# Kernel tuning notes

Measured on AMD Instinct MI355X. Metric: run time of the kernel, lower is better.

The kernel has to match this reference:

```python
import jax, jax.numpy as jnp
import numpy as np

B, S = 1, 8192
QC = 4096          # query_channels
H = 64             # num_heads (== key_channels == output_channels, forced by forward body)
KC = 64            # key_channels
OC = 64            # output_channels
P = 0.25           # dropout prob


def setup_inputs() -> dict:
    key = jax.random.key(0)
    ks = jax.random.split(key, 8)
    w = lambda k, shape: jax.random.normal(k, shape, dtype=jnp.float32) * 0.02
    return {
        "query": jax.random.normal(ks[0], (B, S, QC), dtype=jnp.float32),
        "key_in": jax.random.normal(ks[1], (B, S, KC), dtype=jnp.float32),
        "value": jax.random.normal(ks[2], (B, S, KC), dtype=jnp.float32),
        "mask_u": jax.random.uniform(ks[3], (B, S, H, H), dtype=jnp.float32),
        # Linear weights stored (in, out); torch stores (out, in) but math is identical.
        "Wq": w(ks[4], (QC, H * KC)), "bq": jnp.zeros((H * KC,), jnp.float32),
        "Wk": w(ks[5], (KC, H * KC)), "bk": jnp.zeros((H * KC,), jnp.float32),
        "Wv": w(ks[6], (KC, H * OC)), "bv": jnp.zeros((H * OC,), jnp.float32),
        "Wo": w(ks[7], (H * OC, OC)), "bo": jnp.zeros((OC,), jnp.float32),
    }


def reference(query, key_in, value, mask_u, Wq, bq, Wk, bk, Wv, bv, Wo, bo):
    # Projections
    q = (query @ Wq + bq).reshape(B, S, H, KC)
    k = (key_in @ Wk + bk).reshape(B, S, H, KC)
    v = (value @ Wv + bv).reshape(B, S, H, KC)   # source views v with key_channels (Oc==Kc)
    # transpose(-2, -1): (B, S, KC, H)
    qT = jnp.swapaxes(q, -2, -1)
    kT = jnp.swapaxes(k, -2, -1)
    vT = jnp.swapaxes(v, -2, -1)
    # Per-token 'attention': contracts H of qT against KC of kT (H == KC). No sqrt(d) scale.
    attn_logits = jnp.matmul(qT, kT)             # (B, S, H, H)
    # safe_logsoftmax: numerically stable log-softmax (NOT softmax) over last dim
    attn = jax.nn.log_softmax(attn_logits, axis=-1)
    # dropout p=0.25, deterministic via precomputed uniforms
    keep = (mask_u > P).astype(attn.dtype) / (1.0 - P)
    attn = attn * keep
    out = jnp.matmul(attn, vT)                   # (B, S, H, H)
    # transpose(0,1) -> (S, B, H, H), then view(S, -1) -> (S, B*H*H) with B==1
    out = jnp.swapaxes(out, 0, 1).reshape(S, -1)
    return out @ Wo + bo                          # (S, OC)
```

## Files before the change

### kernel.cpp

```cpp
#include <hip/hip_runtime.h>
#include <stdint.h>
#include <stddef.h>

typedef unsigned short u16;
typedef __bf16 bf16x8 __attribute__((ext_vector_type(8)));
typedef float f32x4 __attribute__((ext_vector_type(4)));

#define DEVINL __device__ __forceinline__

DEVINL u16 f2bf(float f) {
  uint32_t u = __builtin_bit_cast(uint32_t, f);
  u += 0x7FFFu + ((u >> 16) & 1u);
  return (u16)(u >> 16);
}
DEVINL float bf2f(u16 h) {
  uint32_t u = ((uint32_t)h) << 16;
  return __builtin_bit_cast(float, u);
}
DEVINL uint32_t pack2(float a, float b) {
  return (uint32_t)f2bf(a) | ((uint32_t)f2bf(b) << 16);
}

DEVINL void gload_lds16(const u16* g, u16* lds) {
  __builtin_amdgcn_global_load_lds(
      (const __attribute__((address_space(1))) uint32_t*)g,
      (__attribute__((address_space(3))) uint32_t*)lds, 16, 0, 0);
}

__global__ __launch_bounds__(256) void cast_kernel(const float* __restrict__ x,
                                                   u16* __restrict__ y, int n8) {
  int i = blockIdx.x * 256 + threadIdx.x;
  if (i >= n8) return;
  const float4* xp = (const float4*)x + (size_t)i * 2;
  float4 a = xp[0], b = xp[1];
  uint4 o;
  o.x = pack2(a.x, a.y);
  o.y = pack2(a.z, a.w);
  o.z = pack2(b.x, b.y);
  o.w = pack2(b.z, b.w);
  ((uint4*)y)[i] = o;
}

__global__ __launch_bounds__(256) void transpose_cast(const float* __restrict__ W,
                                                      u16* __restrict__ Bt,
                                                      int K, int N) {
  __shared__ float tile[64][65];
  const int nb = blockIdx.x << 6, kb = blockIdx.y << 6;
  const int t = threadIdx.x;
  {
    const int kr = t >> 2, n0 = (t & 3) << 4;
    const float* src = W + (size_t)(kb + kr) * N + nb + n0;
#pragma unroll
    for (int i = 0; i < 16; i += 4) {
      float4 v = *(const float4*)(src + i);
      tile[n0 + i + 0][kr] = v.x;
      tile[n0 + i + 1][kr] = v.y;
      tile[n0 + i + 2][kr] = v.z;
      tile[n0 + i + 3][kr] = v.w;
    }
  }
  __syncthreads();
  {
    const int nr = t >> 2, k0 = (t & 3) << 4;
    u16* dst = Bt + (size_t)(nb + nr) * K + kb + k0;
#pragma unroll
    for (int i = 0; i < 16; i += 8) {
      uint4 o;
      o.x = pack2(tile[nr][k0 + i + 0], tile[nr][k0 + i + 1]);
      o.y = pack2(tile[nr][k0 + i + 2], tile[nr][k0 + i + 3]);
      o.z = pack2(tile[nr][k0 + i + 4], tile[nr][k0 + i + 5]);
      o.w = pack2(tile[nr][k0 + i + 6], tile[nr][k0 + i + 7]);
      *(uint4*)(dst + i) = o;
    }
  }
}

template <int BM, int BN, int WM, int WN, bool OUTF32, bool SPLITK>
__global__ __launch_bounds__(256) void gemm_bf16t(const u16* __restrict__ A,
                                                  const u16* __restrict__ Bt,
                                                  const float* __restrict__ bias,
                                                  void* __restrict__ Cv,
                                                  int M, int N, int K,
                                                  int lda, int ldb) {
  static_assert(WM * WN == 4, "4 waves");
  constexpr int BK = 32;
  constexpr int FM = BM / (WM * 16);
  constexpr int FN = BN / (WN * 16);
  __shared__ __align__(16) u16 Al[BM * BK];
  __shared__ __align__(16) u16 Bl[BN * BK];
  const int t = threadIdx.x;
  const int lane = t & 63, w = t >> 6;
  const int wm = w / WN, wn = w % WN;

  int bn;
  float* Cpart = nullptr;
  if (SPLITK) {
    const int chunk = blockIdx.x;
    A  += (size_t)chunk * K;
    Bt += (size_t)chunk * K;
    Cpart = (float*)Cv + (size_t)chunk * M * N;
    bn = 0;
  } else {
    bn = blockIdx.x * BN;
  }
  const int bm = blockIdx.y * BM;
  const int r16 = lane & 15, khi = lane >> 4;

  f32x4 acc[FM][FN] = {};

  const int srow = t >> 2;
  const int skel = (t & 3) << 3;

  for (int k0 = 0; k0 < K; k0 += BK) {
#pragma unroll
    for (int r = 0; r < BM / 64; ++r) {
      const u16* g = A + (size_t)(bm + r * 64 + srow) * lda + k0 + skel;
      gload_lds16(g, Al + r * 2048 + (w << 9));
    }
#pragma unroll
    for (int r = 0; r < BN / 64; ++r) {
      const u16* g = Bt + (size_t)(bn + r * 64 + srow) * ldb + k0 + skel;
      gload_lds16(g, Bl + r * 2048 + (w << 9));
    }
    __syncthreads();

    bf16x8 af[FM], bfr[FN];
#pragma unroll
    for (int mi = 0; mi < FM; ++mi)
      af[mi] = *(const bf16x8*)(Al + (wm * FM * 16 + mi * 16 + r16) * BK + khi * 8);
#pragma unroll
    for (int ni = 0; ni < FN; ++ni)
      bfr[ni] = *(const bf16x8*)(Bl + (wn * FN * 16 + ni * 16 + r16) * BK + khi * 8);
#pragma unroll
    for (int mi = 0; mi < FM; ++mi)
#pragma unroll
      for (int ni = 0; ni < FN; ++ni)
        acc[mi][ni] = __builtin_amdgcn_mfma_f32_16x16x32_bf16(af[mi], bfr[ni],
                                                              acc[mi][ni], 0, 0, 0);
    __syncthreads();
  }

  const int crow0 = bm + wm * FM * 16 + (khi << 2);
  const int ccol0 = bn + wn * FN * 16 + r16;
#pragma unroll
  for (int mi = 0; mi < FM; ++mi) {
#pragma unroll
    for (int ni = 0; ni < FN; ++ni) {
      const int col = ccol0 + ni * 16;
      const float bv = (!SPLITK && bias) ? bias[col] : 0.0f;
#pragma unroll
      for (int e = 0; e < 4; ++e) {
        const int row = crow0 + mi * 16 + e;
        const float v = acc[mi][ni][e] + bv;
        if (SPLITK)
          Cpart[(size_t)row * N + col] = v;
        else if (OUTF32)
          ((float*)Cv)[(size_t)row * N + col] = v;
        else
          ((u16*)Cv)[(size_t)row * N + col] = f2bf(v);
      }
    }
  }
}

__global__ __launch_bounds__(512, 2) void gemm256(const u16* __restrict__ A,
                                                  const u16* __restrict__ Bt,
                                                  const float* __restrict__ bias,
                                                  u16* __restrict__ C,
                                                  int M, int N, int K) {
  __shared__ __align__(16) u16 LDSu[65536];
  const int t = threadIdx.x;
  const int lane = t & 63, w = t >> 6;
  const int wm = w >> 2, wn = w & 3;
  const int r16 = lane & 15, khi = lane >> 4;
  const int bm = blockIdx.y << 8, bn = blockIdx.x << 8;
  const int nt = K >> 6;

  const int srow = t >> 3;
  const int scb = ((((t & 7) << 4) ^ (((t >> 3) & 7) << 4)) >> 1);

  auto ISSUE_HALF = [&](int tile_, int h_) {
    if (tile_ >= nt) return;
    const int k0_ = tile_ << 6;
    u16* lb_ = LDSu + ((tile_ & 1) << 15) + ((h_ & 2) << 13) + ((h_ & 1) << 13)
               + t * 8;
    const int row0_ = ((h_ & 1) << 7) + srow;
    if (h_ < 2) {
      gload_lds16(A + (size_t)(bm + row0_) * K + k0_ + scb, lb_);
      gload_lds16(A + (size_t)(bm + row0_ + 64) * K + k0_ + scb, lb_ + 4096);
    } else {
      gload_lds16(Bt + (size_t)(bn + row0_) * K + k0_ + scb, lb_);
      gload_lds16(Bt + (size_t)(bn + row0_ + 64) * K + k0_ + scb, lb_ + 4096);
    }
  };

  f32x4 acc[8][4] = {};
  bf16x8 bf[4][2];

  ISSUE_HALF(0, 0);
  ISSUE_HALF(0, 2);
  ISSUE_HALF(0, 3);
  ISSUE_HALF(0, 1);
  ISSUE_HALF(1, 0);
  asm volatile("s_waitcnt vmcnt(4)" ::: "memory");
  __builtin_amdgcn_s_barrier();

  for (int n = 0; n < nt; ++n) {
    const u16* bufb = LDSu + ((n & 1) << 15);
#pragma unroll
    for (int q = 0; q < 4; ++q) {
      bf16x8 af[2][2];
      if (q == 0) {
#pragma unroll
        for (int ni = 0; ni < 4; ++ni)
#pragma unroll
          for (int ks = 0; ks < 2; ++ks)
            bf[ni][ks] = *(const bf16x8*)(bufb + 16384 +
                (64 * wn + 16 * ni + r16) * 64 +
                ((((ks << 6) + (khi << 4)) ^ ((r16 & 7) << 4)) >> 1));
      }
#pragma unroll
      for (int mi2 = 0; mi2 < 2; ++mi2)
#pragma unroll
        for (int ks = 0; ks < 2; ++ks)
          af[mi2][ks] = *(const bf16x8*)(bufb +
              (32 * (2 * q + mi2) + 16 * wm + r16) * 64 +
              ((((ks << 6) + (khi << 4)) ^ ((r16 & 7) << 4)) >> 1));
      __builtin_amdgcn_sched_barrier(0);
      if (q == 0)      ISSUE_HALF(n + 1, 2);
      else if (q == 1) ISSUE_HALF(n + 1, 3);
      else if (q == 2) ISSUE_HALF(n + 1, 1);
      else             ISSUE_HALF(n + 2, 0);
      __builtin_amdgcn_sched_barrier(0);
      __builtin_amdgcn_s_barrier();
      asm volatile("s_waitcnt lgkmcnt(0)" ::: "memory");
      __builtin_amdgcn_sched_barrier(0);
      __builtin_amdgcn_s_setprio(1);
#pragma unroll
      for (int mi2 = 0; mi2 < 2; ++mi2)
#pragma unroll
        for (int ni = 0; ni < 4; ++ni)
#pragma unroll
          for (int ks = 0; ks < 2; ++ks)
            acc[2 * q + mi2][ni] = __builtin_amdgcn_mfma_f32_16x16x32_bf16(
                af[mi2][ks], bf[ni][ks], acc[2 * q + mi2][ni], 0, 0, 0);
      __builtin_amdgcn_s_setprio(0);
      __builtin_amdgcn_sched_barrier(0);
      if (q == 1) {
        if (n < nt - 1)
          asm volatile("s_waitcnt vmcnt(6)" ::: "memory");
        else
          asm volatile("s_waitcnt vmcnt(0)" ::: "memory");
      }
      if (q == 3 && n < nt - 1) {
        if (n < nt - 2)
          asm volatile("s_waitcnt vmcnt(4)" ::: "memory");
        else
          asm volatile("s_waitcnt vmcnt(2)" ::: "memory");
      }
      __builtin_amdgcn_s_barrier();
    }
  }

#pragma unroll
  for (int mi = 0; mi < 8; ++mi) {
    const int row = bm + 32 * mi + 16 * wm + (khi << 2);
#pragma unroll
    for (int ni = 0; ni < 4; ++ni) {
      const int col = bn + 64 * wn + 16 * ni + r16;
      const float bv = bias[col];
#pragma unroll
      for (int e = 0; e < 4; ++e)
        C[(size_t)(row + e) * N + col] = f2bf(acc[mi][ni][e] + bv);
    }
  }
}

__global__ __launch_bounds__(256) void reduce_splitk(const float* __restrict__ part,
                                                     const float* __restrict__ bo,
                                                     float* __restrict__ out, int n) {
  int i = blockIdx.x * 256 + threadIdx.x;
  if (i >= n) return;
  float s = 0.0f;
#pragma unroll
  for (int c = 0; c < 8; ++c) s += part[(size_t)c * 524288 + i];
  out[i] = s + bo[i & 63];
}

__global__ __launch_bounds__(256) void attn_mfma(const u16* __restrict__ Q,
                                                 const u16* __restrict__ Kp,
                                                 const u16* __restrict__ Vp,
                                                 const float* __restrict__ mask,
                                                 u16* __restrict__ OUT) {
  constexpr int LDP = 72;
  __shared__ __align__(16) u16 Pbuf[4][64 * LDP];
  const int t = threadIdx.x;
  const int w = t >> 6, lane = t & 63;
  const int r16 = lane & 15, khi = lane >> 4;
  const int s = blockIdx.x * 4 + w;
  const size_t base = (size_t)s << 12;
  u16* pb = Pbuf[w];

  {
    uint4 rowv[8];
    const uint4* qp = (const uint4*)(Q + base + (size_t)lane * 64);
#pragma unroll
    for (int i = 0; i < 8; ++i) rowv[i] = qp[i];
#pragma unroll
    for (int i = 0; i < 8; ++i) {
      const uint32_t* wp = (const uint32_t*)&rowv[i];
#pragma unroll
      for (int h = 0; h < 4; ++h) {
        uint32_t v = wp[h];
        pb[(8 * i + 2 * h) * LDP + lane] = (u16)(v & 0xffffu);
        pb[(8 * i + 2 * h + 1) * LDP + lane] = (u16)(v >> 16);
      }
    }
  }
  asm volatile("s_waitcnt lgkmcnt(0)" ::: "memory");

  f32x4 acc[4][4] = {};
#pragma unroll
  for (int ks = 0; ks < 2; ++ks) {
    bf16x8 af[4], bfr[4];
#pragma unroll
    for (int mi = 0; mi < 4; ++mi)
      af[mi] = *(const bf16x8*)(pb + (16 * mi + r16) * LDP + ks * 32 + khi * 8);
#pragma unroll
    for (int ni = 0; ni < 4; ++ni)
      bfr[ni] = *(const bf16x8*)(Kp + base + (size_t)(16 * ni + r16) * 64 +
                                 ks * 32 + khi * 8);
#pragma unroll
    for (int mi = 0; mi < 4; ++mi)
#pragma unroll
      for (int ni = 0; ni < 4; ++ni)
        acc[mi][ni] = __builtin_amdgcn_mfma_f32_16x16x32_bf16(af[mi], bfr[ni],
                                                              acc[mi][ni], 0, 0, 0);
  }

  float L[4][4];
#pragma unroll
  for (int mi = 0; mi < 4; ++mi) {
#pragma unroll
    for (int e = 0; e < 4; ++e) {
      float mx = fmaxf(fmaxf(acc[mi][0][e], acc[mi][1][e]),
                       fmaxf(acc[mi][2][e], acc[mi][3][e]));
      mx = fmaxf(mx, __shfl_xor(mx, 1));
      mx = fmaxf(mx, __shfl_xor(mx, 2));
      mx = fmaxf(mx, __shfl_xor(mx, 4));
      mx = fmaxf(mx, __shfl_xor(mx, 8));
      float sm = __expf(acc[mi][0][e] - mx) + __expf(acc[mi][1][e] - mx) +
                 __expf(acc[mi][2][e] - mx) + __expf(acc[mi][3][e] - mx);
      sm += __shfl_xor(sm, 1);
      sm += __shfl_xor(sm, 2);
      sm += __shfl_xor(sm, 4);
      sm += __shfl_xor(sm, 8);
      L[mi][e] = mx + __logf(sm);
    }
  }

  const float* mrow = mask + base;
#pragma unroll
  for (int mi = 0; mi < 4; ++mi) {
#pragma unroll
    for (int ni = 0; ni < 4; ++ni) {
#pragma unroll
      for (int e = 0; e < 4; ++e) {
        const int c = 16 * mi + 4 * khi + e;
        const int j = 16 * ni + r16;
        const float keep = mrow[(size_t)c * 64 + j] > 0.25f ? (1.0f / 0.75f) : 0.0f;
        pb[c * LDP + j] = f2bf((acc[mi][ni][e] - L[mi][e]) * keep);
      }
    }
  }
  asm volatile("s_waitcnt lgkmcnt(0)" ::: "memory");

  f32x4 o[4][4] = {};
#pragma unroll
  for (int ks = 0; ks < 2; ++ks) {
    bf16x8 af[4], bfr[4];
#pragma unroll
    for (int mi = 0; mi < 4; ++mi)
      af[mi] = *(const bf16x8*)(pb + (16 * mi + r16) * LDP + ks * 32 + khi * 8);
#pragma unroll
    for (int ni = 0; ni < 4; ++ni)
      bfr[ni] = *(const bf16x8*)(Vp + base + (size_t)(16 * ni + r16) * 64 +
                                 ks * 32 + khi * 8);
#pragma unroll
    for (int mi = 0; mi < 4; ++mi)
#pragma unroll
      for (int ni = 0; ni < 4; ++ni)
        o[mi][ni] = __builtin_amdgcn_mfma_f32_16x16x32_bf16(af[mi], bfr[ni],
                                                            o[mi][ni], 0, 0, 0);
  }

#pragma unroll
  for (int mi = 0; mi < 4; ++mi) {
#pragma unroll
    for (int ni = 0; ni < 4; ++ni) {
#pragma unroll
      for (int e = 0; e < 4; ++e) {
        const int c = 16 * mi + 4 * khi + e;
        const int jo = 16 * ni + r16;
        OUT[base + (size_t)c * 64 + jo] = f2bf(o[mi][ni][e]);
      }
    }
  }
}

extern "C" void kernel_launch(void* const* d_in, const int* in_sizes, int n_in,
                              void* d_out, int out_size, void* d_ws, size_t ws_size,
                              hipStream_t stream) {
  (void)in_sizes; (void)n_in; (void)out_size; (void)ws_size;
  const float* query  = (const float*)d_in[0];
  const float* key_in = (const float*)d_in[1];
  const float* value  = (const float*)d_in[2];
  const float* mask_u = (const float*)d_in[3];
  const float* Wq = (const float*)d_in[4];
  const float* bq = (const float*)d_in[5];
  const float* Wk = (const float*)d_in[6];
  const float* bk = (const float*)d_in[7];
  const float* Wv = (const float*)d_in[8];
  const float* bv = (const float*)d_in[9];
  const float* Wo = (const float*)d_in[10];
  const float* bo = (const float*)d_in[11];

  char* ws = (char*)d_ws;
  u16* q_bf   = (u16*)(ws + 0);
  u16* WqT    = (u16*)(ws + ((size_t)64 << 20));
  u16* key_bf = (u16*)(ws + ((size_t)96 << 20));
  u16* val_bf = (u16*)(ws + ((size_t)97 << 20));
  u16* WkT    = (u16*)(ws + ((size_t)98 << 20));
  u16* WvT    = (u16*)(ws + ((size_t)98 << 20) + (512 << 10));
  u16* WoT    = (u16*)(ws + ((size_t)99 << 20));
  u16* Qp     = (u16*)(ws + ((size_t)100 << 20));
  u16* Kp     = (u16*)(ws + ((size_t)164 << 20));
  u16* Vp     = (u16*)(ws + ((size_t)228 << 20));
  u16* OUTb   = q_bf;
  float* part = (float*)Kp;

  cast_kernel<<<16384, 256, 0, stream>>>(query, q_bf, 8192 * 4096 / 8);
  cast_kernel<<<256, 256, 0, stream>>>(key_in, key_bf, 8192 * 64 / 8);
  cast_kernel<<<256, 256, 0, stream>>>(value, val_bf, 8192 * 64 / 8);
  transpose_cast<<<dim3(64, 64), 256, 0, stream>>>(Wq, WqT, 4096, 4096);
  transpose_cast<<<dim3(64, 1), 256, 0, stream>>>(Wk, WkT, 64, 4096);
  transpose_cast<<<dim3(64, 1), 256, 0, stream>>>(Wv, WvT, 64, 4096);
  transpose_cast<<<dim3(1, 64), 256, 0, stream>>>(Wo, WoT, 4096, 64);

  gemm256<<<dim3(16, 32), 512, 0, stream>>>(q_bf, WqT, bq, Qp, 8192, 4096, 4096);
  gemm_bf16t<128, 128, 2, 2, false, false>
      <<<dim3(32, 64), 256, 0, stream>>>(key_bf, WkT, bk, Kp, 8192, 4096, 64, 64, 64);
  gemm_bf16t<128, 128, 2, 2, false, false>
      <<<dim3(32, 64), 256, 0, stream>>>(val_bf, WvT, bv, Vp, 8192, 4096, 64, 64, 64);

  attn_mfma<<<2048, 256, 0, stream>>>(Qp, Kp, Vp, mask_u, OUTb);

  gemm_bf16t<128, 64, 4, 1, true, true>
      <<<dim3(8, 64), 256, 0, stream>>>(OUTb, WoT, nullptr, part, 8192, 64, 512, 4096, 4096);
  reduce_splitk<<<2048, 256, 0, stream>>>(part, bo, (float*)d_out, 8192 * 64);
}
```

Baseline: 711.2 us.

## Software-pipeline LDS fragment reads one phase ahead of MFMAs in projection GEMM

Restructures the GEMM main loop so each phase issues LDS reads for the next phase's A fragments (and the next tile's B fragments) before running the current MFMAs. It uses double-buffered register fragments and a loop unrolled by two tiles. The aim is to hide LDS read latency behind matrix-core work instead of waiting on lgkmcnt right before each MFMA block. Register pressure rises, and the vmcnt and barrier placement changes, which could cause races or spills; the unroll by two also assumes an even tile count.

```diff
diff --git a/kernel.cpp b/kernel.cpp
--- a/kernel.cpp
+++ b/kernel.cpp
@@ -194,8 +194,72 @@
     }
   };
 
+  auto LRD = [&](const u16* buf, int row, int ks) -> bf16x8 {
+    return *(const bf16x8*)(buf + row * 64 +
+        ((((ks << 6) + (khi << 4)) ^ ((r16 & 7) << 4)) >> 1));
+  };
+
   f32x4 acc[8][4] = {};
-  bf16x8 bf[4][2];
+  bf16x8 BF0[4][2], BF1[4][2], Pf[2][2], Qf[2][2];
+
+#define AF_ISSUE(AFX, QDST, BUF)                                         \
+  _Pragma("unroll") for (int mi2 = 0; mi2 < 2; ++mi2)                    \
+  _Pragma("unroll") for (int ks = 0; ks < 2; ++ks)                       \
+      AFX[mi2][ks] = LRD(BUF, 32 * (2 * (QDST) + mi2) + 16 * wm + r16, ks);
+
+#define BF_ISSUE(BFX, BUF)                                               \
+  _Pragma("unroll") for (int ni = 0; ni < 4; ++ni)                       \
+  _Pragma("unroll") for (int ks = 0; ks < 2; ++ks)                       \
+      BFX[ni][ks] = LRD((BUF) + 16384, 64 * wn + 16 * ni + r16, ks);
+
+#define MFMA_PHASE(QQ, BFX, AFX)                                         \
+  _Pragma("unroll") for (int mi2 = 0; mi2 < 2; ++mi2)                    \
+  _Pragma("unroll") for (int ni = 0; ni < 4; ++ni)                       \
+  _Pragma("unroll") for (int ks = 0; ks < 2; ++ks)                       \
+      acc[2 * (QQ) + mi2][ni] = __builtin_amdgcn_mfma_f32_16x16x32_bf16( \
+          AFX[mi2][ks], BFX[ni][ks], acc[2 * (QQ) + mi2][ni], 0, 0, 0);
+
+#define SB __builtin_amdgcn_sched_barrier(0)
+
+#define PHASE_HEAD asm volatile("s_waitcnt lgkmcnt(0)" ::: "memory"); SB
+
+#define TILE(NN, BFC, BFN)                                               \
+  {                                                                      \
+    const u16* bufb = LDSu + (((NN) & 1) << 15);                         \
+    const u16* bufn = LDSu + ((((NN) + 1) & 1) << 15);                   \
+                                                                 \
+    PHASE_HEAD;                                                          \
+    AF_ISSUE(Qf, 1, bufb); SB;                                           \
+    ISSUE_HALF((NN) + 1, 2); SB;                                         \
+    __builtin_amdgcn_s_setprio(1); MFMA_PHASE(0, BFC, Pf);               \
+    __builtin_amdgcn_s_setprio(0); SB;                                   \
+    if ((NN) < nt - 1) { asm volatile("s_waitcnt vmcnt(4)" ::: "memory"); } \
+    else               { asm volatile("s_waitcnt vmcnt(0)" ::: "memory"); } \
+    SB; __builtin_amdgcn_s_barrier();                                    \
+                                                                 \
+    PHASE_HEAD;                                                          \
+    AF_ISSUE(Pf, 2, bufb); SB;                                           \
+    ISSUE_HALF((NN) + 1, 3); SB;                                         \
+    __builtin_amdgcn_s_setprio(1); MFMA_PHASE(1, BFC, Qf);               \
+    __builtin_amdgcn_s_setprio(0); SB;                                   \
+    __builtin_amdgcn_s_barrier();                                        \
+                                                                 \
+    PHASE_HEAD;                                                          \
+    AF_ISSUE(Qf, 3, bufb); SB;                                           \
+    ISSUE_HALF((NN) + 1, 1); SB;                                         \
+    __builtin_amdgcn_s_setprio(1); MFMA_PHASE(2, BFC, Pf);               \
+    __builtin_amdgcn_s_setprio(0); SB;                                   \
+    if ((NN) < nt - 1) { asm volatile("s_waitcnt vmcnt(2)" ::: "memory"); } \
+    SB; __builtin_amdgcn_s_barrier();                                    \
+                                                                 \
+    PHASE_HEAD;                                                          \
+    if ((NN) < nt - 1) { BF_ISSUE(BFN, bufn); AF_ISSUE(Pf, 0, bufn); }   \
+    SB;                                                                  \
+    ISSUE_HALF((NN) + 2, 0); SB;                                         \
+    __builtin_amdgcn_s_setprio(1); MFMA_PHASE(3, BFC, Qf);               \
+    __builtin_amdgcn_s_setprio(0); SB;                                   \
+    __builtin_amdgcn_s_barrier();                                        \
+  }
 
   ISSUE_HALF(0, 0);
   ISSUE_HALF(0, 2);
@@ -204,62 +268,14 @@
   ISSUE_HALF(1, 0);
   asm volatile("s_waitcnt vmcnt(4)" ::: "memory");
   __builtin_amdgcn_s_barrier();
-
-  for (int n = 0; n < nt; ++n) {
-    const u16* bufb = LDSu + ((n & 1) << 15);
-#pragma unroll
-    for (int q = 0; q < 4; ++q) {
-      bf16x8 af[2][2];
-      if (q == 0) {
-#pragma unroll
-        for (int ni = 0; ni < 4; ++ni)
-#pragma unroll
-          for (int ks = 0; ks < 2; ++ks)
-            bf[ni][ks] = *(const bf16x8*)(bufb + 16384 +
-                (64 * wn + 16 * ni + r16) * 64 +
-                ((((ks << 6) + (khi << 4)) ^ ((r16 & 7) << 4)) >> 1));
-      }
-#pragma unroll
-      for (int mi2 = 0; mi2 < 2; ++mi2)
-#pragma unroll
-        for (int ks = 0; ks < 2; ++ks)
-          af[mi2][ks] = *(const bf16x8*)(bufb +
-              (32 * (2 * q + mi2) + 16 * wm + r16) * 64 +
-              ((((ks << 6) + (khi << 4)) ^ ((r16 & 7) << 4)) >> 1));
-      __builtin_amdgcn_sched_barrier(0);
-      if (q == 0)      ISSUE_HALF(n + 1, 2);
-      else if (q == 1) ISSUE_HALF(n + 1, 3);
-      else if (q == 2) ISSUE_HALF(n + 1, 1);
-      else             ISSUE_HALF(n + 2, 0);
-      __builtin_amdgcn_sched_barrier(0);
-      __builtin_amdgcn_s_barrier();
-      asm volatile("s_waitcnt lgkmcnt(0)" ::: "memory");
-      __builtin_amdgcn_sched_barrier(0);
-      __builtin_amdgcn_s_setprio(1);
-#pragma unroll
-      for (int mi2 = 0; mi2 < 2; ++mi2)
-#pragma unroll
-        for (int ni = 0; ni < 4; ++ni)
-#pragma unroll
-          for (int ks = 0; ks < 2; ++ks)
-            acc[2 * q + mi2][ni] = __builtin_amdgcn_mfma_f32_16x16x32_bf16(
-                af[mi2][ks], bf[ni][ks], acc[2 * q + mi2][ni], 0, 0, 0);
-      __builtin_amdgcn_s_setprio(0);
-      __builtin_amdgcn_sched_barrier(0);
-      if (q == 1) {
-        if (n < nt - 1)
-          asm volatile("s_waitcnt vmcnt(6)" ::: "memory");
-        else
-          asm volatile("s_waitcnt vmcnt(0)" ::: "memory");
-      }
-      if (q == 3 && n < nt - 1) {
-        if (n < nt - 2)
-          asm volatile("s_waitcnt vmcnt(4)" ::: "memory");
-        else
-          asm volatile("s_waitcnt vmcnt(2)" ::: "memory");
-      }
-      __builtin_amdgcn_s_barrier();
-    }
+  SB;
+  BF_ISSUE(BF0, LDSu);
+  AF_ISSUE(Pf, 0, LDSu);
+  SB;
+
+  for (int n = 0; n < nt; n += 2) {
+    TILE(n, BF0, BF1);
+    TILE(n + 1, BF1, BF0);
   }
 
 #pragma unroll
@@ -274,6 +290,12 @@
         C[(size_t)(row + e) * N + col] = f2bf(acc[mi][ni][e] + bv);
     }
   }
+#undef AF_ISSUE
+#undef BF_ISSUE
+#undef MFMA_PHASE
+#undef SB
+#undef PHASE_HEAD
+#undef TILE
 }
 
 __global__ __launch_bounds__(256) void reduce_splitk(const float* __restrict__ part,
```

Measured after the change: 848.7 us. 19.3% more time.
